# Kernel tuning notes

Measured on AMD Instinct MI355X. Metric: run time of the kernel, lower is better.

The kernel has to match this reference:

```python
import jax, jax.numpy as jnp
import numpy as np

N_NODES = 50000
N_EDGES = 600000
N_GRAPHS = 64
HID = 128
NLAYERS = 4
IN_DIM = 5
NCLS = 5
EPS = 1e-5


def setup_inputs() -> dict:
    key = jax.random.key(0)
    ks = jax.random.split(key, 16)
    x = jax.random.normal(ks[0], (N_NODES, IN_DIM), dtype=jnp.float32)
    edge_index = jax.random.randint(ks[1], (2, N_EDGES), 0, N_NODES, dtype=jnp.int64)
    batch = jnp.sort(jax.random.randint(ks[2], (N_NODES,), 0, N_GRAPHS, dtype=jnp.int64))
    s = 0.05
    Wp = jax.random.normal(ks[3], (IN_DIM, HID), jnp.float32) * s
    bp = jnp.zeros((HID,), jnp.float32)
    Wg = jax.random.normal(ks[4], (NLAYERS, HID, HID), jnp.float32) * s
    bg = jnp.zeros((NLAYERS, HID), jnp.float32)
    gamma = jnp.ones((NLAYERS, HID), jnp.float32)
    beta = jnp.zeros((NLAYERS, HID), jnp.float32)
    W1 = jax.random.normal(ks[5], (2 * HID, HID), jnp.float32) * s
    b1 = jnp.zeros((HID,), jnp.float32)
    W2 = jax.random.normal(ks[6], (HID, HID // 2), jnp.float32) * s
    b2 = jnp.zeros((HID // 2,), jnp.float32)
    W3 = jax.random.normal(ks[7], (HID // 2, NCLS), jnp.float32) * s
    b3 = jnp.zeros((NCLS,), jnp.float32)
    return {"x": x, "edge_index": edge_index, "batch": batch, "Wp": Wp, "bp": bp,
            "Wg": Wg, "bg": bg, "gamma": gamma, "beta": beta,
            "W1": W1, "b1": b1, "W2": W2, "b2": b2, "W3": W3, "b3": b3}


def reference(x, edge_index, batch, Wp, bp, Wg, bg, gamma, beta, W1, b1, W2, b2, W3, b3):
    N = x.shape[0]
    # GCN with added self-loops and symmetric normalization (PyG GCNConv defaults)
    loop = jnp.arange(N)
    src = jnp.concatenate([edge_index[0], loop])
    dst = jnp.concatenate([edge_index[1], loop])
    deg = jax.ops.segment_sum(jnp.ones_like(dst, dtype=x.dtype), dst, num_segments=N)
    dinv = jax.lax.rsqrt(deg)  # deg >= 1 thanks to self-loops
    norm = dinv[src] * dinv[dst]  # [E+N]
    h = x @ Wp + bp  # [N, HID]
    for i in range(NLAYERS):
        m = h @ Wg[i]
        agg = jax.ops.segment_sum(m[src] * norm[:, None], dst, num_segments=N) + bg[i]
        # BatchNorm1d (training-mode stats over nodes)
        mu = jnp.mean(agg, axis=0)
        var = jnp.var(agg, axis=0)
        h = gamma[i] * (agg - mu) * jax.lax.rsqrt(var + EPS) + beta[i]
        h = jax.nn.relu(h)  # dropout is identity in eval mode
    # mean_max global pooling per graph
    cnt = jax.ops.segment_sum(jnp.ones((N,), h.dtype), batch, num_segments=N_GRAPHS)
    x_mean = jax.ops.segment_sum(h, batch, num_segments=N_GRAPHS) / jnp.maximum(cnt, 1.0)[:, None]
    x_max = jax.ops.segment_max(h, batch, num_segments=N_GRAPHS)
    x_max = jnp.where(jnp.isfinite(x_max), x_max, 0.0)
    pooled = jnp.concatenate([x_mean, x_max], axis=1)  # [B, 2*HID]
    h1 = jax.nn.relu(pooled @ W1 + b1)
    h2 = jax.nn.relu(h1 @ W2 + b2)
    return h2 @ W3 + b3  # [B, num_classes]
```

## Files before the change

kernel.cpp:

```cpp
#include <hip/hip_runtime.h>
#include <hip/hip_bf16.h>

#define N_NODES 50000
#define N_EDGES 600000
#define N_GRAPHS 64
#define HID 128
#define NLAYERS 4
#define IN_DIM 5
#define NCLS 5
#define EPS 1e-5f
#define SCAN_BLK ((N_NODES + 511) / 512)
#define POOL_CHUNKS 16
#define HLS 132
#define BSLOT 64
#define WS 136

typedef __attribute__((ext_vector_type(8))) short s16x8;
typedef __attribute__((ext_vector_type(4))) float f32x4;

__device__ __forceinline__ unsigned short f2bf(float x) {
    unsigned u = __float_as_uint(x);
    unsigned r = (u + 0x7fffu + ((u >> 16) & 1u)) >> 16;
    return (unsigned short)r;
}
__device__ __forceinline__ float2 bfpair(unsigned u) {
    float2 r;
    r.x = __uint_as_float(u << 16);
    r.y = __uint_as_float(u & 0xffff0000u);
    return r;
}
__device__ __forceinline__ float bf2f(unsigned short s) {
    return __uint_as_float(((unsigned)s) << 16);
}


__global__ void k_count(const int* __restrict__ dst, int* __restrict__ cnt) {
    int i = blockIdx.x * blockDim.x + threadIdx.x;
    if (i < N_EDGES) atomicAdd(&cnt[dst[i]], 1);
}

__global__ void k_scan1(const int* __restrict__ cnt, int* __restrict__ rp, int* __restrict__ bsum) {
    __shared__ int s[512];
    int t = threadIdx.x;
    int i = blockIdx.x * 512 + t;
    int v = (i < N_NODES) ? cnt[i] : 0;
    s[t] = v;
    __syncthreads();
    for (int off = 1; off < 512; off <<= 1) {
        int x = (t >= off) ? s[t - off] : 0;
        __syncthreads();
        s[t] += x;
        __syncthreads();
    }
    if (i < N_NODES) rp[i + 1] = s[t];
    if (t == 511) bsum[blockIdx.x] = s[511];
}

__global__ void k_scan2g(int* __restrict__ bsum, const int* __restrict__ batch,
                         int* __restrict__ gstart) {
    if (blockIdx.x == 0) {
        __shared__ int s[128];
        int t = threadIdx.x;
        int v = (t < SCAN_BLK) ? bsum[t] : 0;
        s[t] = v;
        __syncthreads();
        for (int off = 1; off < 128; off <<= 1) {
            int x = (t >= off) ? s[t - off] : 0;
            __syncthreads();
            s[t] += x;
            __syncthreads();
        }
        if (t < SCAN_BLK) bsum[t] = s[t] - v;
    } else {
        int t = threadIdx.x;
        if (t <= N_GRAPHS) {
            int lo = 0, hi = N_NODES;
            while (lo < hi) {
                int mid = (lo + hi) >> 1;
                if (batch[mid] < t) lo = mid + 1; else hi = mid;
            }
            gstart[t] = lo;
        }
    }
}

__global__ void k_scan3d(int* __restrict__ rp, const int* __restrict__ bsum,
                         const int* __restrict__ cnt, float* __restrict__ dinv) {
    int i = blockIdx.x * 512 + threadIdx.x;
    if (i < N_NODES) {
        rp[i + 1] += bsum[blockIdx.x];
        dinv[i] = rsqrtf((float)(cnt[i] + 1));
    }
    if (i == 0) rp[0] = 0;
}

__global__ void k_fill(const int* __restrict__ src, const int* __restrict__ dst,
                       const int* __restrict__ rp, int* __restrict__ cursor,
                       int2* __restrict__ cw, const float* __restrict__ dinv) {
    int e = blockIdx.x * blockDim.x + threadIdx.x;
    if (e < N_EDGES) {
        int d = dst[e];
        int pos = atomicAdd(&cursor[d], 1);
        int s = src[e];
        int2 p;
        p.x = s;
        p.y = __float_as_int(dinv[s]);
        cw[rp[d] + pos] = p;
    }
}


__global__ __launch_bounds__(256) void k_gemm0(const float* __restrict__ x,
                                               const float* __restrict__ Wp,
                                               const float* __restrict__ bp,
                                               const float* __restrict__ W,
                                               unsigned short* __restrict__ Bm) {
    __shared__ float Wl[HID * 64];
    __shared__ float Hl[64 * HLS];
    __shared__ float xl[64 * IN_DIM];
    __shared__ float Wpl[IN_DIM * HID];
    __shared__ float bpl[HID];
    int t = threadIdx.x;
    int half = blockIdx.x & 1;
    int f0 = half * 64;
    {
        const float4* Wg4 = (const float4*)W;
        float4* Wl4 = (float4*)Wl;
        for (int idx = t; idx < HID * 16; idx += 256) {
            int k = idx >> 4, c = idx & 15;
            Wl4[idx] = Wg4[k * 32 + (f0 >> 2) + c];
        }
    }
    for (int idx = t; idx < IN_DIM * HID; idx += 256) Wpl[idx] = Wp[idx];
    if (t < HID) bpl[t] = bp[t];
    int fg = t & 15;
    int ng = t >> 4;
    int fl = fg * 4;
    const int numTiles = (N_NODES + 63) / 64;
    int stride = gridDim.x >> 1;
    for (int tile = blockIdx.x >> 1; tile < numTiles; tile += stride) {
        int n0 = tile * 64;
        __syncthreads();
        for (int idx = t; idx < 64 * IN_DIM; idx += 256) {
            int g = n0 * IN_DIM + idx;
            xl[idx] = (g < N_NODES * IN_DIM) ? x[g] : 0.f;
        }
        __syncthreads();
        for (int idx = t; idx < 64 * HID; idx += 256) {
            int n = idx >> 7, k = idx & 127;
            float acc = bpl[k];
#pragma unroll
            for (int j = 0; j < IN_DIM; j++) acc += xl[n * IN_DIM + j] * Wpl[j * HID + k];
            Hl[n * HLS + k] = acc;
        }
        __syncthreads();
        float acc[4][4];
#pragma unroll
        for (int j = 0; j < 4; j++)
#pragma unroll
            for (int c = 0; c < 4; c++) acc[j][c] = 0.f;
        for (int k = 0; k < HID; k += 4) {
            float4 w0 = *(const float4*)&Wl[(k + 0) * 64 + fl];
            float4 w1 = *(const float4*)&Wl[(k + 1) * 64 + fl];
            float4 w2 = *(const float4*)&Wl[(k + 2) * 64 + fl];
            float4 w3 = *(const float4*)&Wl[(k + 3) * 64 + fl];
#pragma unroll
            for (int j = 0; j < 4; j++) {
                float4 hv = *(const float4*)&Hl[(ng * 4 + j) * HLS + k];
                acc[j][0] += hv.x * w0.x + hv.y * w1.x + hv.z * w2.x + hv.w * w3.x;
                acc[j][1] += hv.x * w0.y + hv.y * w1.y + hv.z * w2.y + hv.w * w3.y;
                acc[j][2] += hv.x * w0.z + hv.y * w1.z + hv.z * w2.z + hv.w * w3.z;
                acc[j][3] += hv.x * w0.w + hv.y * w1.w + hv.z * w2.w + hv.w * w3.w;
            }
        }
#pragma unroll
        for (int j = 0; j < 4; j++) {
            int n = n0 + ng * 4 + j;
            if (n < N_NODES) {
                ushort4 o;
                o.x = f2bf(acc[j][0]);
                o.y = f2bf(acc[j][1]);
                o.z = f2bf(acc[j][2]);
                o.w = f2bf(acc[j][3]);
                *(ushort4*)&Bm[(size_t)n * HID + f0 + fl] = o;
            }
        }
    }
}


__global__ __launch_bounds__(256) void k_gemmM(const unsigned short* __restrict__ Abf,
                                               const float* __restrict__ W,
                                               unsigned short* __restrict__ Bm,
                                               const float* __restrict__ scale,
                                               const float* __restrict__ shift) {
    __shared__ unsigned short Wt[HID * WS];
    __shared__ unsigned short Al[64 * WS];
    int t = threadIdx.x;
    for (int idx = t; idx < HID * HID; idx += 256) {
        int k = idx >> 7, n = idx & 127;
        Wt[n * WS + k] = f2bf(W[idx]);
    }
    int lane = t & 63, wv = t >> 6;
    int rbase = (wv & 1) * 32;
    int cbase = (wv >> 1) * 64;
    int mr = lane & 15, q = lane >> 4;
    const int numTiles = (N_NODES + 63) / 64;
    for (int tile = blockIdx.x; tile < numTiles; tile += gridDim.x) {
        int n0 = tile * 64;
        __syncthreads();
        {
            const uint2* Ag = (const uint2*)(Abf + (size_t)n0 * HID);
            int limRow = min(64, N_NODES - n0);
            for (int idx = t; idx < 64 * 32; idx += 256) {
                int row = idx >> 5, c4 = idx & 31;
                uint2 u = (row < limRow) ? Ag[row * 32 + c4] : make_uint2(0u, 0u);
                float2 ab = bfpair(u.x);
                float2 cd = bfpair(u.y);
                int kf = c4 * 4;
                float4 sc = *(const float4*)&scale[kf];
                float4 sh = *(const float4*)&shift[kf];
                float v0 = fmaxf(ab.x * sc.x + sh.x, 0.f);
                float v1 = fmaxf(ab.y * sc.y + sh.y, 0.f);
                float v2 = fmaxf(cd.x * sc.z + sh.z, 0.f);
                float v3 = fmaxf(cd.y * sc.w + sh.w, 0.f);
                unsigned lo = (unsigned)f2bf(v0) | ((unsigned)f2bf(v1) << 16);
                unsigned hi = (unsigned)f2bf(v2) | ((unsigned)f2bf(v3) << 16);
                *(uint2*)&Al[row * WS + kf] = make_uint2(lo, hi);
            }
        }
        __syncthreads();
        f32x4 acc[2][4];
#pragma unroll
        for (int rt = 0; rt < 2; rt++)
#pragma unroll
            for (int ct = 0; ct < 4; ct++) acc[rt][ct] = (f32x4){0.f, 0.f, 0.f, 0.f};
#pragma unroll
        for (int kk = 0; kk < HID; kk += 32) {
            s16x8 a0 = *(const s16x8*)&Al[(rbase + mr) * WS + kk + q * 8];
            s16x8 a1 = *(const s16x8*)&Al[(rbase + 16 + mr) * WS + kk + q * 8];
#pragma unroll
            for (int ct = 0; ct < 4; ct++) {
                s16x8 b = *(const s16x8*)&Wt[(cbase + ct * 16 + mr) * WS + kk + q * 8];
                acc[0][ct] = __builtin_amdgcn_mfma_f32_16x16x32_bf16(a0, b, acc[0][ct], 0, 0, 0);
                acc[1][ct] = __builtin_amdgcn_mfma_f32_16x16x32_bf16(a1, b, acc[1][ct], 0, 0, 0);
            }
        }
#pragma unroll
        for (int rt = 0; rt < 2; rt++)
#pragma unroll
            for (int ct = 0; ct < 4; ct++)
#pragma unroll
                for (int r = 0; r < 4; r++) {
                    int node = n0 + rbase + rt * 16 + q * 4 + r;
                    if (node < N_NODES) {
                        int f = cbase + ct * 16 + mr;
                        Bm[(size_t)node * HID + f] = f2bf(acc[rt][ct][r]);
                    }
                }
    }
}


__global__ __launch_bounds__(256) void k_gather(const unsigned int* __restrict__ Bmu,
                                                const int* __restrict__ rp,
                                                const int2* __restrict__ cw,
                                                const float* __restrict__ dinv,
                                                const float* __restrict__ bg,
                                                unsigned short* __restrict__ Aout,
                                                float* __restrict__ psum,
                                                float* __restrict__ psq) {
    __shared__ float ls[4 * HID], lq[4 * HID];
    int wave = threadIdx.x >> 6;
    int lane = threadIdx.x & 63;
    int v = blockIdx.x * 4 + wave;
    int beg = rp[v], end = rp[v + 1];
    float dv = dinv[v];
    float2 self = bfpair(Bmu[(size_t)v * 64 + lane]);
    float2 acc = make_float2(self.x * dv, self.y * dv);
    int e = beg;
    for (; e + 3 < end; e += 4) {
        int2 p0 = cw[e];
        int2 p1 = cw[e + 1];
        int2 p2 = cw[e + 2];
        int2 p3 = cw[e + 3];
        unsigned u0 = Bmu[(size_t)p0.x * 64 + lane];
        unsigned u1 = Bmu[(size_t)p1.x * 64 + lane];
        unsigned u2 = Bmu[(size_t)p2.x * 64 + lane];
        unsigned u3 = Bmu[(size_t)p3.x * 64 + lane];
        float2 m0 = bfpair(u0);
        float2 m1 = bfpair(u1);
        float2 m2 = bfpair(u2);
        float2 m3 = bfpair(u3);
        float w0 = __int_as_float(p0.y), w1 = __int_as_float(p1.y);
        float w2 = __int_as_float(p2.y), w3 = __int_as_float(p3.y);
        acc.x += m0.x * w0 + m1.x * w1 + m2.x * w2 + m3.x * w3;
        acc.y += m0.y * w0 + m1.y * w1 + m2.y * w2 + m3.y * w3;
    }
    for (; e < end; e++) {
        int2 p = cw[e];
        float2 m = bfpair(Bmu[(size_t)p.x * 64 + lane]);
        float w = __int_as_float(p.y);
        acc.x += m.x * w;
        acc.y += m.y * w;
    }
    int f = lane * 2;
    ushort2 o;
    o.x = f2bf(acc.x * dv + bg[f]);
    o.y = f2bf(acc.y * dv + bg[f + 1]);
    ((ushort2*)Aout)[(size_t)v * 64 + lane] = o;
    float vx = bf2f(o.x), vy = bf2f(o.y);
    ls[wave * HID + f] = vx;
    ls[wave * HID + f + 1] = vy;
    lq[wave * HID + f] = vx * vx;
    lq[wave * HID + f + 1] = vy * vy;
    __syncthreads();
    int tt = threadIdx.x;
    if (tt < HID) {
        float s = ls[tt] + ls[HID + tt] + ls[2 * HID + tt] + ls[3 * HID + tt];
        float s2 = lq[tt] + lq[HID + tt] + lq[2 * HID + tt] + lq[3 * HID + tt];
        int slot = blockIdx.x & (BSLOT - 1);
        atomicAdd(&psum[slot * HID + tt], s);
        atomicAdd(&psq[slot * HID + tt], s2);
    }
}


__global__ __launch_bounds__(128) void k_bnfin(float* __restrict__ psum,
                                               float* __restrict__ psq,
                                               const float* __restrict__ gamma,
                                               const float* __restrict__ beta,
                                               float* __restrict__ scale,
                                               float* __restrict__ shift) {
    int f = threadIdx.x;
    float s = 0.f, s2 = 0.f;
#pragma unroll 8
    for (int b = 0; b < BSLOT; b++) {
        s += psum[b * HID + f];
        s2 += psq[b * HID + f];
    }
#pragma unroll 8
    for (int b = 0; b < BSLOT; b++) {
        psum[b * HID + f] = 0.f;
        psq[b * HID + f] = 0.f;
    }
    const float invN = 1.f / (float)N_NODES;
    float mu = s * invN;
    float var = s2 * invN - mu * mu;
    float rs = rsqrtf(var + EPS) * gamma[f];
    scale[f] = rs;
    shift[f] = beta[f] - mu * rs;
}


__global__ __launch_bounds__(128) void k_pool(const unsigned short* __restrict__ A,
                                              const float* __restrict__ scale,
                                              const float* __restrict__ shift,
                                              const int* __restrict__ gstart,
                                              float* __restrict__ poolPart) {
    int g = blockIdx.x;
    int c = blockIdx.y;
    int f = threadIdx.x;
    int beg = gstart[g], end = gstart[g + 1];
    int len = end - beg;
    int per = (len + POOL_CHUNKS - 1) / POOL_CHUNKS;
    int s0 = beg + c * per;
    int s1 = min(s0 + per, end);
    float sc = scale[f], sh = shift[f];
    float sa = 0.f, sb = 0.f, ma = 0.f, mb = 0.f;
    int n = s0;
    for (; n + 1 < s1; n += 2) {
        float v0 = bf2f(A[(size_t)n * HID + f]);
        float v1 = bf2f(A[(size_t)(n + 1) * HID + f]);
        v0 = fmaxf(v0 * sc + sh, 0.f);
        v1 = fmaxf(v1 * sc + sh, 0.f);
        sa += v0; ma = fmaxf(ma, v0);
        sb += v1; mb = fmaxf(mb, v1);
    }
    if (n < s1) {
        float v = fmaxf(bf2f(A[(size_t)n * HID + f]) * sc + sh, 0.f);
        sa += v; ma = fmaxf(ma, v);
    }
    poolPart[((size_t)g * POOL_CHUNKS + c) * 256 + f] = sa + sb;
    poolPart[((size_t)g * POOL_CHUNKS + c) * 256 + 128 + f] = fmaxf(ma, mb);
}


__global__ __launch_bounds__(128) void k_head(const float* __restrict__ poolPart,
                                              const int* __restrict__ gstart,
                                              const float* __restrict__ W1, const float* __restrict__ b1,
                                              const float* __restrict__ W2, const float* __restrict__ b2,
                                              const float* __restrict__ W3, const float* __restrict__ b3,
                                              float* __restrict__ out) {
    __shared__ float pl[2 * HID];
    __shared__ float h1[HID];
    __shared__ float h2[HID / 2];
    int g = blockIdx.x, t = threadIdx.x;
    float cnt = fmaxf((float)(gstart[g + 1] - gstart[g]), 1.f);
    float s = 0.f, mx = 0.f;
#pragma unroll
    for (int c = 0; c < POOL_CHUNKS; c++) {
        const float* p = &poolPart[((size_t)g * POOL_CHUNKS + c) * 256];
        s += p[t];
        mx = fmaxf(mx, p[128 + t]);
    }
    pl[t] = s / cnt;
    pl[HID + t] = mx;
    __syncthreads();
    float acc = b1[t];
    for (int k = 0; k < 2 * HID; k++) acc += pl[k] * W1[k * HID + t];
    h1[t] = fmaxf(acc, 0.f);
    __syncthreads();
    if (t < HID / 2) {
        float a2 = b2[t];
        for (int k = 0; k < HID; k++) a2 += h1[k] * W2[k * (HID / 2) + t];
        h2[t] = fmaxf(a2, 0.f);
    }
    __syncthreads();
    if (t < NCLS) {
        float a3 = b3[t];
        for (int k = 0; k < HID / 2; k++) a3 += h2[k] * W3[k * NCLS + t];
        out[g * NCLS + t] = a3;
    }
}

extern "C" void kernel_launch(void* const* d_in, const int* in_sizes, int n_in,
                              void* d_out, int out_size, void* d_ws, size_t ws_size,
                              hipStream_t stream) {
    const float* x     = (const float*)d_in[0];
    const int*   ei    = (const int*)d_in[1];
    const int*   batch = (const int*)d_in[2];
    const float* Wp    = (const float*)d_in[3];
    const float* bp    = (const float*)d_in[4];
    const float* Wg    = (const float*)d_in[5];
    const float* bg    = (const float*)d_in[6];
    const float* gamma = (const float*)d_in[7];
    const float* beta  = (const float*)d_in[8];
    const float* W1    = (const float*)d_in[9];
    const float* b1    = (const float*)d_in[10];
    const float* W2    = (const float*)d_in[11];
    const float* b2    = (const float*)d_in[12];
    const float* W3    = (const float*)d_in[13];
    const float* b3    = (const float*)d_in[14];
    const int* src = ei;
    const int* dst = ei + N_EDGES;
    float* out = (float*)d_out;

    char* base = (char*)d_ws;
    size_t off = 0;
    auto alloc = [&](size_t bytes) -> void* {
        void* p = base + off;
        off += (bytes + 255) & ~(size_t)255;
        return p;
    };
    int*   counts = (int*)alloc((size_t)N_NODES * 4);
    int*   cursor = (int*)alloc((size_t)N_NODES * 4);
    float* psum   = (float*)alloc((size_t)BSLOT * HID * 4);
    float* psq    = (float*)alloc((size_t)BSLOT * HID * 4);
    size_t zeroBytes = off;
    int*   rp      = (int*)alloc((size_t)(N_NODES + 1) * 4);
    int*   bsum    = (int*)alloc(128 * 4);
    int2*  cw      = (int2*)alloc((size_t)N_EDGES * 8);
    float* dinv    = (float*)alloc((size_t)N_NODES * 4);
    float* scaleA  = (float*)alloc((size_t)NLAYERS * HID * 4);
    float* shiftA  = (float*)alloc((size_t)NLAYERS * HID * 4);
    int*   gstart  = (int*)alloc((size_t)(N_GRAPHS + 1) * 4);
    float* poolPart= (float*)alloc((size_t)N_GRAPHS * POOL_CHUNKS * 256 * 4);
    unsigned short* A = (unsigned short*)alloc((size_t)N_NODES * HID * 2);
    unsigned short* B = (unsigned short*)alloc((size_t)N_NODES * HID * 2);
    (void)ws_size; (void)in_sizes; (void)n_in; (void)out_size;

    hipMemsetAsync(d_ws, 0, zeroBytes, stream);

    k_count<<<(N_EDGES + 255) / 256, 256, 0, stream>>>(dst, counts);
    k_scan1<<<SCAN_BLK, 512, 0, stream>>>(counts, rp, bsum);
    k_scan2g<<<2, 128, 0, stream>>>(bsum, batch, gstart);
    k_scan3d<<<SCAN_BLK, 512, 0, stream>>>(rp, bsum, counts, dinv);
    k_fill<<<(N_EDGES + 255) / 256, 256, 0, stream>>>(src, dst, rp, cursor, cw, dinv);

    for (int i = 0; i < NLAYERS; i++) {
        if (i == 0) {
            k_gemm0<<<1024, 256, 0, stream>>>(x, Wp, bp, Wg, B);
        } else {
            k_gemmM<<<768, 256, 0, stream>>>(A, Wg + (size_t)i * HID * HID, B,
                                             scaleA + (i - 1) * HID, shiftA + (i - 1) * HID);
        }
        k_gather<<<N_NODES / 4, 256, 0, stream>>>((const unsigned int*)B, rp, cw, dinv,
                                                  bg + i * HID, A, psum, psq);
        k_bnfin<<<1, 128, 0, stream>>>(psum, psq, gamma + i * HID, beta + i * HID,
                                       scaleA + i * HID, shiftA + i * HID);
    }
    dim3 pg(N_GRAPHS, POOL_CHUNKS);
    k_pool<<<pg, 128, 0, stream>>>(A, scaleA + 3 * HID, shiftA + 3 * HID, gstart, poolPart);
    k_head<<<N_GRAPHS, 128, 0, stream>>>(poolPart, gstart, W1, b1, W2, b2, W3, b3, out);
}
```

Measured before the change: 450.2 us.

## Merge layer-0 GEMM into MFMA kernel and split gather wave into edge halves

The layer-0 projection GEMM, previously a separate fp32 CUDA-core kernel, now goes through the bf16 MFMA k_gemmM path. The input projection x@Wp+bp is computed in-kernel into the bf16 A tile. The gather kernel now splits each wave into two 32-lane halves that process alternate edges with 8-byte loads, then combines them via a cross-lane shuffle. This gives more memory parallelism per node and wider loads, at the cost of an extra shuffle reduction and rounding the layer-0 input to bf16.

```diff
diff --git a/kernel.cpp b/kernel.cpp
--- a/kernel.cpp
+++ b/kernel.cpp
@@ -11,7 +11,6 @@
 #define EPS 1e-5f
 #define SCAN_BLK ((N_NODES + 511) / 512)
 #define POOL_CHUNKS 16
-#define HLS 132
 #define BSLOT 64
 #define WS 136
 
@@ -110,96 +109,28 @@
 }
 
 
-__global__ __launch_bounds__(256) void k_gemm0(const float* __restrict__ x,
+__global__ __launch_bounds__(256) void k_gemmM(const unsigned short* __restrict__ Abf,
+                                               const float* __restrict__ x,
                                                const float* __restrict__ Wp,
                                                const float* __restrict__ bp,
                                                const float* __restrict__ W,
-                                               unsigned short* __restrict__ Bm) {
-    __shared__ float Wl[HID * 64];
-    __shared__ float Hl[64 * HLS];
-    __shared__ float xl[64 * IN_DIM];
+                                               unsigned short* __restrict__ Bm,
+                                               const float* __restrict__ scale,
+                                               const float* __restrict__ shift,
+                                               int layer0) {
+    __shared__ unsigned short Wt[HID * WS];
+    __shared__ unsigned short Al[64 * WS];
     __shared__ float Wpl[IN_DIM * HID];
     __shared__ float bpl[HID];
-    int t = threadIdx.x;
-    int half = blockIdx.x & 1;
-    int f0 = half * 64;
-    {
-        const float4* Wg4 = (const float4*)W;
-        float4* Wl4 = (float4*)Wl;
-        for (int idx = t; idx < HID * 16; idx += 256) {
-            int k = idx >> 4, c = idx & 15;
-            Wl4[idx] = Wg4[k * 32 + (f0 >> 2) + c];
-        }
-    }
-    for (int idx = t; idx < IN_DIM * HID; idx += 256) Wpl[idx] = Wp[idx];
-    if (t < HID) bpl[t] = bp[t];
-    int fg = t & 15;
-    int ng = t >> 4;
-    int fl = fg * 4;
-    const int numTiles = (N_NODES + 63) / 64;
-    int stride = gridDim.x >> 1;
-    for (int tile = blockIdx.x >> 1; tile < numTiles; tile += stride) {
-        int n0 = tile * 64;
-        __syncthreads();
-        for (int idx = t; idx < 64 * IN_DIM; idx += 256) {
-            int g = n0 * IN_DIM + idx;
-            xl[idx] = (g < N_NODES * IN_DIM) ? x[g] : 0.f;
-        }
-        __syncthreads();
-        for (int idx = t; idx < 64 * HID; idx += 256) {
-            int n = idx >> 7, k = idx & 127;
-            float acc = bpl[k];
-#pragma unroll
-            for (int j = 0; j < IN_DIM; j++) acc += xl[n * IN_DIM + j] * Wpl[j * HID + k];
-            Hl[n * HLS + k] = acc;
-        }
-        __syncthreads();
-        float acc[4][4];
-#pragma unroll
-        for (int j = 0; j < 4; j++)
-#pragma unroll
-            for (int c = 0; c < 4; c++) acc[j][c] = 0.f;
-        for (int k = 0; k < HID; k += 4) {
-            float4 w0 = *(const float4*)&Wl[(k + 0) * 64 + fl];
-            float4 w1 = *(const float4*)&Wl[(k + 1) * 64 + fl];
-            float4 w2 = *(const float4*)&Wl[(k + 2) * 64 + fl];
-            float4 w3 = *(const float4*)&Wl[(k + 3) * 64 + fl];
-#pragma unroll
-            for (int j = 0; j < 4; j++) {
-                float4 hv = *(const float4*)&Hl[(ng * 4 + j) * HLS + k];
-                acc[j][0] += hv.x * w0.x + hv.y * w1.x + hv.z * w2.x + hv.w * w3.x;
-                acc[j][1] += hv.x * w0.y + hv.y * w1.y + hv.z * w2.y + hv.w * w3.y;
-                acc[j][2] += hv.x * w0.z + hv.y * w1.z + hv.z * w2.z + hv.w * w3.z;
-                acc[j][3] += hv.x * w0.w + hv.y * w1.w + hv.z * w2.w + hv.w * w3.w;
-            }
-        }
-#pragma unroll
-        for (int j = 0; j < 4; j++) {
-            int n = n0 + ng * 4 + j;
-            if (n < N_NODES) {
-                ushort4 o;
-                o.x = f2bf(acc[j][0]);
-                o.y = f2bf(acc[j][1]);
-                o.z = f2bf(acc[j][2]);
-                o.w = f2bf(acc[j][3]);
-                *(ushort4*)&Bm[(size_t)n * HID + f0 + fl] = o;
-            }
-        }
-    }
-}
-
-
-__global__ __launch_bounds__(256) void k_gemmM(const unsigned short* __restrict__ Abf,
-                                               const float* __restrict__ W,
-                                               unsigned short* __restrict__ Bm,
-                                               const float* __restrict__ scale,
-                                               const float* __restrict__ shift) {
-    __shared__ unsigned short Wt[HID * WS];
-    __shared__ unsigned short Al[64 * WS];
+    __shared__ float xl[64 * IN_DIM];
     int t = threadIdx.x;
     for (int idx = t; idx < HID * HID; idx += 256) {
         int k = idx >> 7, n = idx & 127;
         Wt[n * WS + k] = f2bf(W[idx]);
+    }
+    if (layer0) {
+        for (int idx = t; idx < IN_DIM * HID; idx += 256) Wpl[idx] = Wp[idx];
+        if (t < HID) bpl[t] = bp[t];
     }
     int lane = t & 63, wv = t >> 6;
     int rbase = (wv & 1) * 32;
@@ -209,7 +140,20 @@
     for (int tile = blockIdx.x; tile < numTiles; tile += gridDim.x) {
         int n0 = tile * 64;
         __syncthreads();
-        {
+        if (layer0) {
+            for (int idx = t; idx < 64 * IN_DIM; idx += 256) {
+                int g = n0 * IN_DIM + idx;
+                xl[idx] = (g < N_NODES * IN_DIM) ? x[g] : 0.f;
+            }
+            __syncthreads();
+            for (int idx = t; idx < 64 * HID; idx += 256) {
+                int n = idx >> 7, k = idx & 127;
+                float acc = bpl[k];
+#pragma unroll
+                for (int j = 0; j < IN_DIM; j++) acc += xl[n * IN_DIM + j] * Wpl[j * HID + k];
+                Al[n * WS + k] = f2bf(acc);
+            }
+        } else {
             const uint2* Ag = (const uint2*)(Abf + (size_t)n0 * HID);
             int limRow = min(64, N_NODES - n0);
             for (int idx = t; idx < 64 * 32; idx += 256) {
@@ -262,7 +206,7 @@
 }
 
 
-__global__ __launch_bounds__(256) void k_gather(const unsigned int* __restrict__ Bmu,
+__global__ __launch_bounds__(256) void k_gather(const uint2* __restrict__ Bm2,
                                                 const int* __restrict__ rp,
                                                 const int2* __restrict__ cw,
                                                 const float* __restrict__ dinv,
@@ -273,55 +217,70 @@
     __shared__ float ls[4 * HID], lq[4 * HID];
     int wave = threadIdx.x >> 6;
     int lane = threadIdx.x & 63;
+    int s = lane & 31;
+    int p = lane >> 5;
     int v = blockIdx.x * 4 + wave;
     int beg = rp[v], end = rp[v + 1];
     float dv = dinv[v];
-    float2 self = bfpair(Bmu[(size_t)v * 64 + lane]);
-    float2 acc = make_float2(self.x * dv, self.y * dv);
-    int e = beg;
-    for (; e + 3 < end; e += 4) {
-        int2 p0 = cw[e];
-        int2 p1 = cw[e + 1];
-        int2 p2 = cw[e + 2];
-        int2 p3 = cw[e + 3];
-        unsigned u0 = Bmu[(size_t)p0.x * 64 + lane];
-        unsigned u1 = Bmu[(size_t)p1.x * 64 + lane];
-        unsigned u2 = Bmu[(size_t)p2.x * 64 + lane];
-        unsigned u3 = Bmu[(size_t)p3.x * 64 + lane];
-        float2 m0 = bfpair(u0);
-        float2 m1 = bfpair(u1);
-        float2 m2 = bfpair(u2);
-        float2 m3 = bfpair(u3);
-        float w0 = __int_as_float(p0.y), w1 = __int_as_float(p1.y);
-        float w2 = __int_as_float(p2.y), w3 = __int_as_float(p3.y);
-        acc.x += m0.x * w0 + m1.x * w1 + m2.x * w2 + m3.x * w3;
-        acc.y += m0.y * w0 + m1.y * w1 + m2.y * w2 + m3.y * w3;
-    }
-    for (; e < end; e++) {
-        int2 p = cw[e];
-        float2 m = bfpair(Bmu[(size_t)p.x * 64 + lane]);
-        float w = __int_as_float(p.y);
-        acc.x += m.x * w;
-        acc.y += m.y * w;
-    }
-    int f = lane * 2;
-    ushort2 o;
-    o.x = f2bf(acc.x * dv + bg[f]);
-    o.y = f2bf(acc.y * dv + bg[f + 1]);
-    ((ushort2*)Aout)[(size_t)v * 64 + lane] = o;
-    float vx = bf2f(o.x), vy = bf2f(o.y);
-    ls[wave * HID + f] = vx;
-    ls[wave * HID + f + 1] = vy;
-    lq[wave * HID + f] = vx * vx;
-    lq[wave * HID + f + 1] = vy * vy;
+    float4 acc = make_float4(0.f, 0.f, 0.f, 0.f);
+    if (p == 0) {
+        uint2 u = Bm2[(size_t)v * 32 + s];
+        float2 lo = bfpair(u.x), hi = bfpair(u.y);
+        acc.x = lo.x * dv; acc.y = lo.y * dv; acc.z = hi.x * dv; acc.w = hi.y * dv;
+    }
+    int e = beg + p;
+    for (; e + 2 < end; e += 4) {
+        int2 pe0 = cw[e];
+        int2 pe1 = cw[e + 2];
+        uint2 u0 = Bm2[(size_t)pe0.x * 32 + s];
+        uint2 u1 = Bm2[(size_t)pe1.x * 32 + s];
+        float w0 = __int_as_float(pe0.y);
+        float w1 = __int_as_float(pe1.y);
+        float2 l0 = bfpair(u0.x), h0 = bfpair(u0.y);
+        float2 l1 = bfpair(u1.x), h1 = bfpair(u1.y);
+        acc.x += l0.x * w0 + l1.x * w1;
+        acc.y += l0.y * w0 + l1.y * w1;
+        acc.z += h0.x * w0 + h1.x * w1;
+        acc.w += h0.y * w0 + h1.y * w1;
+    }
+    if (e < end) {
+        int2 pe = cw[e];
+        uint2 u = Bm2[(size_t)pe.x * 32 + s];
+        float w = __int_as_float(pe.y);
+        float2 lo = bfpair(u.x), hi = bfpair(u.y);
+        acc.x += lo.x * w; acc.y += lo.y * w; acc.z += hi.x * w; acc.w += hi.y * w;
+    }
+    acc.x += __shfl_xor(acc.x, 32);
+    acc.y += __shfl_xor(acc.y, 32);
+    acc.z += __shfl_xor(acc.z, 32);
+    acc.w += __shfl_xor(acc.w, 32);
+    int f = s * 4;
+    if (p == 0) {
+        float4 bgv = *(const float4*)&bg[f];
+        ushort4 o;
+        o.x = f2bf(acc.x * dv + bgv.x);
+        o.y = f2bf(acc.y * dv + bgv.y);
+        o.z = f2bf(acc.z * dv + bgv.z);
+        o.w = f2bf(acc.w * dv + bgv.w);
+        *(ushort4*)&Aout[(size_t)v * HID + f] = o;
+        float vx = bf2f(o.x), vy = bf2f(o.y), vz = bf2f(o.z), vw = bf2f(o.w);
+        ls[wave * HID + f + 0] = vx;
+        ls[wave * HID + f + 1] = vy;
+        ls[wave * HID + f + 2] = vz;
+        ls[wave * HID + f + 3] = vw;
+        lq[wave * HID + f + 0] = vx * vx;
+        lq[wave * HID + f + 1] = vy * vy;
+        lq[wave * HID + f + 2] = vz * vz;
+        lq[wave * HID + f + 3] = vw * vw;
+    }
     __syncthreads();
     int tt = threadIdx.x;
     if (tt < HID) {
-        float s = ls[tt] + ls[HID + tt] + ls[2 * HID + tt] + ls[3 * HID + tt];
-        float s2 = lq[tt] + lq[HID + tt] + lq[2 * HID + tt] + lq[3 * HID + tt];
+        float ssum = ls[tt] + ls[HID + tt] + ls[2 * HID + tt] + ls[3 * HID + tt];
+        float ssq = lq[tt] + lq[HID + tt] + lq[2 * HID + tt] + lq[3 * HID + tt];
         int slot = blockIdx.x & (BSLOT - 1);
-        atomicAdd(&psum[slot * HID + tt], s);
-        atomicAdd(&psq[slot * HID + tt], s2);
+        atomicAdd(&psum[slot * HID + tt], ssum);
+        atomicAdd(&psq[slot * HID + tt], ssq);
     }
 }
 
@@ -479,13 +438,11 @@
     k_fill<<<(N_EDGES + 255) / 256, 256, 0, stream>>>(src, dst, rp, cursor, cw, dinv);
 
     for (int i = 0; i < NLAYERS; i++) {
-        if (i == 0) {
-            k_gemm0<<<1024, 256, 0, stream>>>(x, Wp, bp, Wg, B);
-        } else {
-            k_gemmM<<<768, 256, 0, stream>>>(A, Wg + (size_t)i * HID * HID, B,
-                                             scaleA + (i - 1) * HID, shiftA + (i - 1) * HID);
-        }
-        k_gather<<<N_NODES / 4, 256, 0, stream>>>((const unsigned int*)B, rp, cw, dinv,
+        k_gemmM<<<768, 256, 0, stream>>>(A, x, Wp, bp, Wg + (size_t)i * HID * HID, B,
+                                         scaleA + ((i == 0) ? 0 : (i - 1)) * HID,
+                                         shiftA + ((i == 0) ? 0 : (i - 1)) * HID,
+                                         (i == 0) ? 1 : 0);
+        k_gather<<<N_NODES / 4, 256, 0, stream>>>((const uint2*)B, rp, cw, dinv,
                                                   bg + i * HID, A, psum, psq);
         k_bnfin<<<1, 128, 0, stream>>>(psum, psq, gamma + i * HID, beta + i * HID,
                                        scaleA + i * HID, shiftA + i * HID);
```

Result: faster. 435.5 us (-3.3%).
